# Performance work log

Measured on AMD Instinct MI355X. Metric: run time of the kernel, lower is better.

The kernel has to match this reference:

```python
import jax, jax.numpy as jnp
import numpy as np

STRIDE, PADDING, EPS = 2, 1, 1e-5


def setup_inputs() -> dict:
    key = jax.random.key(0)
    k1, k2, k3 = jax.random.split(key, 3)
    C_in, C_out, K = 64, 64, 4
    x = jax.random.normal(k1, (32, C_in, 64, 64), dtype=jnp.float32)
    weight = jax.random.normal(k2, (C_in, C_out, K, K), dtype=jnp.float32) * 0.05  # torch layout (in,out,kh,kw)
    conv_bias = jax.random.normal(k3, (C_out,), dtype=jnp.float32) * 0.02
    gamma = jnp.ones((C_out,), dtype=jnp.float32)
    beta = jnp.zeros((C_out,), dtype=jnp.float32)
    running_mean = jnp.zeros((C_out,), dtype=jnp.float32)
    running_var = jnp.ones((C_out,), dtype=jnp.float32)
    return {"x": x, "weight": weight, "conv_bias": conv_bias, "gamma": gamma,
            "beta": beta, "running_mean": running_mean, "running_var": running_var}


def _conv_transpose2d(x, weight, bias, stride, padding):
    # torch.nn.functional.conv_transpose2d equivalent:
    # conv with lhs_dilation=stride, spatially-flipped kernel, in/out axes swapped,
    # and padding k-1-p on each side.
    k = weight.shape[2]
    w_t = jnp.transpose(jnp.flip(weight, (2, 3)), (1, 0, 2, 3))  # (Cout, Cin, k, k)
    pad = k - 1 - padding
    y = jax.lax.conv_general_dilated(
        x, w_t,
        window_strides=(1, 1),
        padding=[(pad, pad), (pad, pad)],
        lhs_dilation=(stride, stride),
        dimension_numbers=("NCHW", "OIHW", "NCHW"),
    )
    return y + bias[None, :, None, None]


def reference(x, weight, conv_bias, gamma, beta, running_mean, running_var):
    # ConvTranspose2d
    y = _conv_transpose2d(x, weight, conv_bias, STRIDE, PADDING)  # [N,C,128,128]
    # BatchNorm2d (inference, running stats)
    scale = gamma * jax.lax.rsqrt(running_var + EPS)
    y = (y - running_mean[None, :, None, None]) * scale[None, :, None, None] + beta[None, :, None, None]
    # Softmax over channel dim
    y = jax.nn.softmax(y, axis=1)
    # MaxPool2d(k=2, s=2): H,W are even, so reshape-max is exact
    N, C, H, W = y.shape
    y = y.reshape(N, C, H // 2, 2, W // 2, 2).max(axis=(3, 5))  # [N,C,64,64]
    return y
```

## Files before the change

### kernel.cpp

```cpp
#include <hip/hip_runtime.h>
#include <hip/hip_bf16.h>
#include <math.h>


typedef __attribute__((ext_vector_type(8))) short short8;
typedef __attribute__((ext_vector_type(4))) float floatx4;

#define COLS 66

__device__ ushort g_wfrag[4 * 8 * 4 * 64 * 8];
__device__ float g_aff[64];

__device__ __forceinline__ ushort f2bf(float f) {
  union { float f; unsigned u; } v; v.f = f;
  unsigned r = v.u + 0x7FFF + ((v.u >> 16) & 1);
  return (ushort)(r >> 16);
}

__global__ __launch_bounds__(256) void prep_kernel(
    const float* __restrict__ w, const float* __restrict__ bias,
    const float* __restrict__ gamma, const float* __restrict__ beta,
    const float* __restrict__ mean, const float* __restrict__ var) {
  int t = blockIdx.x * 256 + threadIdx.x;
  int cin0 = (t >> 6) * 2;
  int cout = t & 63;
  int nt = cout >> 4, b15 = cout & 15;
  int q = (cin0 & 31) >> 3;
  int j = cin0 & 7;
  int ksq = cin0 >> 5;
  float A = gamma[cout] * rsqrtf(var[cout] + 1e-5f);

  const float4* p0 = (const float4*)&w[(cin0 * 64 + cout) * 16];
  const float4* p1 = (const float4*)&w[((cin0 + 1) * 64 + cout) * 16];
  float a[16], b[16];
  {
    float4 f0 = p0[0], f1 = p0[1], f2 = p0[2], f3 = p0[3];
    a[0]=f0.x; a[1]=f0.y; a[2]=f0.z; a[3]=f0.w; a[4]=f1.x; a[5]=f1.y; a[6]=f1.z; a[7]=f1.w;
    a[8]=f2.x; a[9]=f2.y; a[10]=f2.z; a[11]=f2.w; a[12]=f3.x; a[13]=f3.y; a[14]=f3.z; a[15]=f3.w;
    float4 g0 = p1[0], g1 = p1[1], g2 = p1[2], g3 = p1[3];
    b[0]=g0.x; b[1]=g0.y; b[2]=g0.z; b[3]=g0.w; b[4]=g1.x; b[5]=g1.y; b[6]=g1.z; b[7]=g1.w;
    b[8]=g2.x; b[9]=g2.y; b[10]=g2.z; b[11]=g2.w; b[12]=g3.x; b[13]=g3.y; b[14]=g3.z; b[15]=g3.w;
  }
#pragma unroll
  for (int kh = 0; kh < 4; ++kh)
#pragma unroll
    for (int kw = 0; kw < 4; ++kw) {
      int r = (kh & 1) ? 0 : 1;
      int pp = (kw & 1) ? 0 : 1;
      int c = r * 2 + pp;
      int tap = (kh >> 1) * 2 + (kw >> 1);
      int ks = tap * 2 + ksq;
      unsigned u = (unsigned)f2bf(a[kh * 4 + kw] * A) |
                   ((unsigned)f2bf(b[kh * 4 + kw] * A) << 16);
      *(unsigned*)&g_wfrag[(((c * 8 + ks) * 4 + nt) * 64 + q * 16 + b15) * 8 + j] = u;
    }

  if (t < 64) {
    float Ai = gamma[t] * rsqrtf(var[t] + 1e-5f);
    g_aff[t] = (bias[t] - mean[t]) * Ai + beta[t];
  }
}

__global__ __launch_bounds__(256, 4) void fused_kernel(const float* __restrict__ x,
                                                       float* __restrict__ out) {
  __shared__ ushort xs[4 * COLS * 64];

  const int tid  = threadIdx.x;
  const int ph0  = blockIdx.x * 2;
  const int n    = blockIdx.y;
  const int wave = tid >> 6;
  const int lane = tid & 63;
  const int b15  = lane & 15;
  const int q    = lane >> 4;
  const int wr   = wave >> 1;
  const int wc   = wave & 1;

  for (int e = tid; e < 4 * 16 * 16; e += 256) {
    int iw4 = e & 15;
    int c4  = (e >> 4) & 15;
    int row = e >> 8;
    int ih  = ph0 - 1 + row;
    float4 v0 = {0.f, 0.f, 0.f, 0.f}, v1 = v0, v2 = v0, v3 = v0;
    if (ih >= 0 && ih < 64) {
      const float* xp = x + ((n * 64 + c4 * 4) * 64 + ih) * 64 + iw4 * 4;
      v0 = *(const float4*)xp;          v1 = *(const float4*)(xp + 4096);
      v2 = *(const float4*)(xp + 8192); v3 = *(const float4*)(xp + 12288);
    }
    int chunk = c4 >> 1, half4 = (c4 & 1) * 4;
    float cc[4][4] = {{v0.x, v1.x, v2.x, v3.x}, {v0.y, v1.y, v2.y, v3.y},
                      {v0.z, v1.z, v2.z, v3.z}, {v0.w, v1.w, v2.w, v3.w}};
#pragma unroll
    for (int ii = 0; ii < 4; ++ii) {
      int col = iw4 * 4 + ii + 1;
      __hip_bfloat162 lo = __float22bfloat162_rn({cc[ii][0], cc[ii][1]});
      __hip_bfloat162 hi = __float22bfloat162_rn({cc[ii][2], cc[ii][3]});
      ushort4 pk = {*(ushort*)&lo.x, *(ushort*)&lo.y, *(ushort*)&hi.x, *(ushort*)&hi.y};
      *(ushort4*)&xs[(row * COLS + col) * 64 + ((chunk ^ (col & 7)) * 8) + half4] = pk;
    }
  }
  for (int e = tid; e < 4 * 2 * 16; e += 256) {
    int c4 = e & 15, side = (e >> 4) & 1, row = e >> 5;
    int col = side ? 65 : 0;
    int chunk = c4 >> 1, half4 = (c4 & 1) * 4;
    ushort4 z; z.x = z.y = z.z = z.w = 0;
    *(ushort4*)&xs[(row * COLS + col) * 64 + ((chunk ^ (col & 7)) * 8) + half4] = z;
  }
  __syncthreads();

  float Dc[4];
#pragma unroll
  for (int nt = 0; nt < 4; ++nt) Dc[nt] = g_aff[nt * 16 + b15];

  floatx4 pooled[8];
#pragma unroll
  for (int i = 0; i < 8; ++i) pooled[i] = (floatx4){0.f, 0.f, 0.f, 0.f};

  short8 bfA[4], bfB[4];
  {
    const short8* wf = (const short8*)g_wfrag;
#pragma unroll
    for (int nt = 0; nt < 4; ++nt) bfA[nt] = wf[nt * 64 + lane];
  }

  for (int c = 0; c < 4; ++c) {
    const int r = c >> 1, p = c & 1;
    floatx4 acc[8];
#pragma unroll
    for (int i = 0; i < 8; ++i) acc[i] = (floatx4){0.f, 0.f, 0.f, 0.f};

#pragma unroll
    for (int ks = 0; ks < 8; ++ks) {
      short8* cur = (ks & 1) ? bfB : bfA;
      short8* nxt = (ks & 1) ? bfA : bfB;
      if (ks < 7) {
        const short8* wf = (const short8*)g_wfrag + (c * 8 + ks + 1) * 256;
#pragma unroll
        for (int nt = 0; nt < 4; ++nt) nxt[nt] = wf[nt * 64 + lane];
      } else if (c < 3) {
        const short8* wf = (const short8*)g_wfrag + (c + 1) * 8 * 256;
#pragma unroll
        for (int nt = 0; nt < 4; ++nt) nxt[nt] = wf[nt * 64 + lane];
      }
      const int a = ks >> 2, b = (ks >> 1) & 1;
      const int hrow = wr + (r ? (a ? 1 : 2) : (a ? 0 : 1));
      const int dx   = p ? (b ? 0 : 1) : (b ? -1 : 0);
      const int chunk = (ks & 1) * 4 + q;
      short8 af[2];
#pragma unroll
      for (int mt = 0; mt < 2; ++mt) {
        int col = wc * 32 + mt * 16 + b15 + dx + 1;
        af[mt] = *(const short8*)&xs[(hrow * COLS + col) * 64 + ((chunk ^ (col & 7)) * 8)];
      }
#pragma unroll
      for (int nt = 0; nt < 4; ++nt)
#pragma unroll
        for (int mt = 0; mt < 2; ++mt)
          acc[mt * 4 + nt] =
              __builtin_amdgcn_mfma_f32_16x16x32_bf16(af[mt], cur[nt], acc[mt * 4 + nt], 0, 0, 0);
    }

#pragma unroll
    for (int mt = 0; mt < 2; ++mt) {
      float sm[4] = {0.f, 0.f, 0.f, 0.f};
#pragma unroll
      for (int nt = 0; nt < 4; ++nt)
#pragma unroll
        for (int reg = 0; reg < 4; ++reg) {
          float e = __expf(acc[mt * 4 + nt][reg] + Dc[nt]);
          acc[mt * 4 + nt][reg] = e;
          sm[reg] += e;
        }
#pragma unroll
      for (int reg = 0; reg < 4; ++reg) {
        sm[reg] += __shfl_xor(sm[reg], 1, 64);
        sm[reg] += __shfl_xor(sm[reg], 2, 64);
        sm[reg] += __shfl_xor(sm[reg], 4, 64);
        sm[reg] += __shfl_xor(sm[reg], 8, 64);
        sm[reg] = 1.0f / sm[reg];
      }
#pragma unroll
      for (int nt = 0; nt < 4; ++nt)
#pragma unroll
        for (int reg = 0; reg < 4; ++reg)
          pooled[mt * 4 + nt][reg] =
              fmaxf(pooled[mt * 4 + nt][reg], acc[mt * 4 + nt][reg] * sm[reg]);
    }
  }

  __syncthreads();
  float* red = (float*)xs;
#pragma unroll
  for (int mt = 0; mt < 2; ++mt)
#pragma unroll
    for (int nt = 0; nt < 4; ++nt)
#pragma unroll
      for (int reg = 0; reg < 4; ++reg)
        red[(wr * 64 + nt * 16 + b15) * 66 + wc * 32 + mt * 16 + q * 4 + reg] =
            pooled[mt * 4 + nt][reg];
  __syncthreads();
  for (int e = tid; e < 4096; e += 256) {
    int pw2  = e & 31;
    int cout = (e >> 5) & 63;
    int rl   = e >> 11;
    float2 val = *(float2*)&red[(rl * 64 + cout) * 66 + pw2 * 2];
    *(float2*)&out[((n * 64 + cout) * 64 + (ph0 + rl)) * 64 + pw2 * 2] = val;
  }
}

extern "C" void kernel_launch(void* const* d_in, const int* in_sizes, int n_in,
                              void* d_out, int out_size, void* d_ws, size_t ws_size,
                              hipStream_t stream) {
  const float* x     = (const float*)d_in[0];
  const float* w     = (const float*)d_in[1];
  const float* bias  = (const float*)d_in[2];
  const float* gamma = (const float*)d_in[3];
  const float* beta  = (const float*)d_in[4];
  const float* mean  = (const float*)d_in[5];
  const float* var   = (const float*)d_in[6];
  float* out = (float*)d_out;

  prep_kernel<<<8, 256, 0, stream>>>(w, bias, gamma, beta, mean, var);
  dim3 grid(32, 32);
  fused_kernel<<<grid, 256, 0, stream>>>(x, out);
}
```

Before: 120.4 us.

## Split parity classes across waves, one pooled row per block, atomic LDS max

Each block now handles one pooled output row with 8 waves, and each wave pair owns one of the four output parity classes instead of looping over them. Max pooling across waves goes through workgroup-scoped float atomic max in LDS. Edge columns are masked rather than padded. Several smaller changes come with it: log2(e) is folded into the weights and affine term so exp2 can be used, DPP replaces the shuffle reductions, a native bf16 pack conversion is used, and the bias is preloaded into the accumulators. The aim is more parallelism and less serial per-wave work, at the cost of LDS atomics and more redundant input staging per output row.

```diff
diff --git a/kernel.cpp b/kernel.cpp
--- a/kernel.cpp
+++ b/kernel.cpp
@@ -5,11 +5,13 @@
 
 typedef __attribute__((ext_vector_type(8))) short short8;
 typedef __attribute__((ext_vector_type(4))) float floatx4;
-
-#define COLS 66
+typedef __attribute__((ext_vector_type(2))) unsigned uint2v;
+typedef __attribute__((ext_vector_type(4))) unsigned uint4v;
 
 __device__ ushort g_wfrag[4 * 8 * 4 * 64 * 8];
 __device__ float g_aff[64];
+
+#define L2E 1.44269504088896340736f
 
 __device__ __forceinline__ ushort f2bf(float f) {
   union { float f; unsigned u; } v; v.f = f;
@@ -28,7 +30,7 @@
   int q = (cin0 & 31) >> 3;
   int j = cin0 & 7;
   int ksq = cin0 >> 5;
-  float A = gamma[cout] * rsqrtf(var[cout] + 1e-5f);
+  float Aw = gamma[cout] * rsqrtf(var[cout] + 1e-5f) * L2E;
 
   const float4* p0 = (const float4*)&w[(cin0 * 64 + cout) * 16];
   const float4* p1 = (const float4*)&w[((cin0 + 1) * 64 + cout) * 16];
@@ -50,36 +52,80 @@
       int c = r * 2 + pp;
       int tap = (kh >> 1) * 2 + (kw >> 1);
       int ks = tap * 2 + ksq;
-      unsigned u = (unsigned)f2bf(a[kh * 4 + kw] * A) |
-                   ((unsigned)f2bf(b[kh * 4 + kw] * A) << 16);
+      unsigned u = (unsigned)f2bf(a[kh * 4 + kw] * Aw) |
+                   ((unsigned)f2bf(b[kh * 4 + kw] * Aw) << 16);
       *(unsigned*)&g_wfrag[(((c * 8 + ks) * 4 + nt) * 64 + q * 16 + b15) * 8 + j] = u;
     }
 
   if (t < 64) {
-    float Ai = gamma[t] * rsqrtf(var[t] + 1e-5f);
-    g_aff[t] = (bias[t] - mean[t]) * Ai + beta[t];
-  }
-}
-
-__global__ __launch_bounds__(256, 4) void fused_kernel(const float* __restrict__ x,
+    float A0 = gamma[t] * rsqrtf(var[t] + 1e-5f);
+    g_aff[t] = ((bias[t] - mean[t]) * A0 + beta[t]) * L2E;
+  }
+}
+
+__device__ __forceinline__ unsigned cvtpk(float a, float b) {
+  unsigned r;
+  asm("v_cvt_pk_bf16_f32 %0, %1, %2" : "=v"(r) : "v"(a), "v"(b));
+  return r;
+}
+
+__device__ __forceinline__ short8 and8(short8 v, unsigned m) {
+  union { short8 s; uint4v u; } x;
+  x.s = v;
+  x.u &= m;
+  return x.s;
+}
+
+template <int CTRL>
+__device__ __forceinline__ float dpp_add(float v) {
+  unsigned t = (unsigned)__builtin_amdgcn_update_dpp(
+      0, (int)__float_as_uint(v), CTRL, 0xF, 0xF, true);
+  return v + __uint_as_float(t);
+}
+
+__device__ __forceinline__ float sum16(float v) {
+  v = dpp_add<0xB1>(v);
+  v = dpp_add<0x4E>(v);
+  v = dpp_add<0x141>(v);
+  v = dpp_add<0x140>(v);
+  return v;
+}
+
+__device__ __forceinline__ float fexp2(float x) {
+#if __has_builtin(__builtin_amdgcn_exp2f)
+  return __builtin_amdgcn_exp2f(x);
+#else
+  return exp2f(x);
+#endif
+}
+
+__global__ __launch_bounds__(512, 6) void fused_kernel(const float* __restrict__ x,
                                                        float* __restrict__ out) {
-  __shared__ ushort xs[4 * COLS * 64];
+  __shared__ __align__(16) ushort xs[3 * 64 * 64];
+  __shared__ __align__(16) float red[64 * 64];
 
   const int tid  = threadIdx.x;
-  const int ph0  = blockIdx.x * 2;
+  const int ph   = blockIdx.x;
   const int n    = blockIdx.y;
   const int wave = tid >> 6;
   const int lane = tid & 63;
   const int b15  = lane & 15;
   const int q    = lane >> 4;
-  const int wr   = wave >> 1;
   const int wc   = wave & 1;
-
-  for (int e = tid; e < 4 * 16 * 16; e += 256) {
+  const int c    = wave >> 1;
+  const int r    = c >> 1, p = c & 1;
+
+  {
+    float4 z = {0.f, 0.f, 0.f, 0.f};
+    *(float4*)&red[tid * 8] = z;
+    *(float4*)&red[tid * 8 + 4] = z;
+  }
+
+  for (int e = tid; e < 768; e += 512) {
     int iw4 = e & 15;
     int c4  = (e >> 4) & 15;
     int row = e >> 8;
-    int ih  = ph0 - 1 + row;
+    int ih  = ph - 1 + row;
     float4 v0 = {0.f, 0.f, 0.f, 0.f}, v1 = v0, v2 = v0, v3 = v0;
     if (ih >= 0 && ih < 64) {
       const float* xp = x + ((n * 64 + c4 * 4) * 64 + ih) * 64 + iw4 * 4;
@@ -91,119 +137,99 @@
                       {v0.z, v1.z, v2.z, v3.z}, {v0.w, v1.w, v2.w, v3.w}};
 #pragma unroll
     for (int ii = 0; ii < 4; ++ii) {
-      int col = iw4 * 4 + ii + 1;
-      __hip_bfloat162 lo = __float22bfloat162_rn({cc[ii][0], cc[ii][1]});
-      __hip_bfloat162 hi = __float22bfloat162_rn({cc[ii][2], cc[ii][3]});
-      ushort4 pk = {*(ushort*)&lo.x, *(ushort*)&lo.y, *(ushort*)&hi.x, *(ushort*)&hi.y};
-      *(ushort4*)&xs[(row * COLS + col) * 64 + ((chunk ^ (col & 7)) * 8) + half4] = pk;
-    }
-  }
-  for (int e = tid; e < 4 * 2 * 16; e += 256) {
-    int c4 = e & 15, side = (e >> 4) & 1, row = e >> 5;
-    int col = side ? 65 : 0;
-    int chunk = c4 >> 1, half4 = (c4 & 1) * 4;
-    ushort4 z; z.x = z.y = z.z = z.w = 0;
-    *(ushort4*)&xs[(row * COLS + col) * 64 + ((chunk ^ (col & 7)) * 8) + half4] = z;
-  }
-  __syncthreads();
+      int col = iw4 * 4 + ii;
+      uint2v pk = {cvtpk(cc[ii][0], cc[ii][1]), cvtpk(cc[ii][2], cc[ii][3])};
+      *(uint2v*)&xs[(row * 64 + col) * 64 + ((chunk ^ (col & 7)) * 8) + half4] = pk;
+    }
+  }
 
   float Dc[4];
 #pragma unroll
   for (int nt = 0; nt < 4; ++nt) Dc[nt] = g_aff[nt * 16 + b15];
 
-  floatx4 pooled[8];
-#pragma unroll
-  for (int i = 0; i < 8; ++i) pooled[i] = (floatx4){0.f, 0.f, 0.f, 0.f};
+  const unsigned m_b0 = (p == 1 && wc == 1 && b15 == 15) ? 0u : ~0u;
+  const unsigned m_b1 = (p == 0 && wc == 0 && b15 == 0) ? 0u : ~0u;
+
+  int A_[2][2][2];
+#pragma unroll
+  for (int mt = 0; mt < 2; ++mt)
+#pragma unroll
+    for (int b = 0; b < 2; ++b) {
+      int col = (wc * 32 + mt * 16 + b15 + (b ? p - 1 : p)) & 63;
+#pragma unroll
+      for (int par = 0; par < 2; ++par)
+        A_[mt][b][par] = r * 4096 + col * 64 + (((par * 4 + q) ^ (col & 7)) * 8);
+    }
 
   short8 bfA[4], bfB[4];
   {
-    const short8* wf = (const short8*)g_wfrag;
+    const short8* wf = (const short8*)g_wfrag + (c * 8) * 256;
 #pragma unroll
     for (int nt = 0; nt < 4; ++nt) bfA[nt] = wf[nt * 64 + lane];
   }
-
-  for (int c = 0; c < 4; ++c) {
-    const int r = c >> 1, p = c & 1;
-    floatx4 acc[8];
-#pragma unroll
-    for (int i = 0; i < 8; ++i) acc[i] = (floatx4){0.f, 0.f, 0.f, 0.f};
-
-#pragma unroll
-    for (int ks = 0; ks < 8; ++ks) {
-      short8* cur = (ks & 1) ? bfB : bfA;
-      short8* nxt = (ks & 1) ? bfA : bfB;
-      if (ks < 7) {
-        const short8* wf = (const short8*)g_wfrag + (c * 8 + ks + 1) * 256;
-#pragma unroll
-        for (int nt = 0; nt < 4; ++nt) nxt[nt] = wf[nt * 64 + lane];
-      } else if (c < 3) {
-        const short8* wf = (const short8*)g_wfrag + (c + 1) * 8 * 256;
-#pragma unroll
-        for (int nt = 0; nt < 4; ++nt) nxt[nt] = wf[nt * 64 + lane];
+  __syncthreads();
+
+  floatx4 acc[8];
+#pragma unroll
+  for (int nt = 0; nt < 4; ++nt) {
+    acc[nt]     = (floatx4){Dc[nt], Dc[nt], Dc[nt], Dc[nt]};
+    acc[4 + nt] = (floatx4){Dc[nt], Dc[nt], Dc[nt], Dc[nt]};
+  }
+
+#pragma unroll
+  for (int ks = 0; ks < 8; ++ks) {
+    const int a = ks >> 2, b = (ks >> 1) & 1, par = ks & 1;
+    short8* cur = (ks & 1) ? bfB : bfA;
+    short8* nxt = (ks & 1) ? bfA : bfB;
+    if (ks < 7) {
+      const short8* wf = (const short8*)g_wfrag + (c * 8 + ks + 1) * 256;
+#pragma unroll
+      for (int nt = 0; nt < 4; ++nt) nxt[nt] = wf[nt * 64 + lane];
+    }
+    const int ho = a ? 0 : 4096;
+    short8 af0 = *(const short8*)&xs[A_[0][b][par] + ho];
+    short8 af1 = *(const short8*)&xs[A_[1][b][par] + ho];
+    if (b == 0) af1 = and8(af1, m_b0);
+    else        af0 = and8(af0, m_b1);
+#pragma unroll
+    for (int nt = 0; nt < 4; ++nt) {
+      acc[nt]     = __builtin_amdgcn_mfma_f32_16x16x32_bf16(af0, cur[nt], acc[nt], 0, 0, 0);
+      acc[4 + nt] = __builtin_amdgcn_mfma_f32_16x16x32_bf16(af1, cur[nt], acc[4 + nt], 0, 0, 0);
+    }
+  }
+
+#pragma unroll
+  for (int mt = 0; mt < 2; ++mt) {
+    float sm[4] = {0.f, 0.f, 0.f, 0.f};
+#pragma unroll
+    for (int nt = 0; nt < 4; ++nt)
+#pragma unroll
+      for (int reg = 0; reg < 4; ++reg) {
+        float e = fexp2(acc[mt * 4 + nt][reg]);
+        acc[mt * 4 + nt][reg] = e;
+        sm[reg] += e;
       }
-      const int a = ks >> 2, b = (ks >> 1) & 1;
-      const int hrow = wr + (r ? (a ? 1 : 2) : (a ? 0 : 1));
-      const int dx   = p ? (b ? 0 : 1) : (b ? -1 : 0);
-      const int chunk = (ks & 1) * 4 + q;
-      short8 af[2];
-#pragma unroll
-      for (int mt = 0; mt < 2; ++mt) {
-        int col = wc * 32 + mt * 16 + b15 + dx + 1;
-        af[mt] = *(const short8*)&xs[(hrow * COLS + col) * 64 + ((chunk ^ (col & 7)) * 8)];
-      }
-#pragma unroll
-      for (int nt = 0; nt < 4; ++nt)
-#pragma unroll
-        for (int mt = 0; mt < 2; ++mt)
-          acc[mt * 4 + nt] =
-              __builtin_amdgcn_mfma_f32_16x16x32_bf16(af[mt], cur[nt], acc[mt * 4 + nt], 0, 0, 0);
-    }
-
-#pragma unroll
-    for (int mt = 0; mt < 2; ++mt) {
-      float sm[4] = {0.f, 0.f, 0.f, 0.f};
-#pragma unroll
-      for (int nt = 0; nt < 4; ++nt)
-#pragma unroll
-        for (int reg = 0; reg < 4; ++reg) {
-          float e = __expf(acc[mt * 4 + nt][reg] + Dc[nt]);
-          acc[mt * 4 + nt][reg] = e;
-          sm[reg] += e;
-        }
-#pragma unroll
-      for (int reg = 0; reg < 4; ++reg) {
-        sm[reg] += __shfl_xor(sm[reg], 1, 64);
-        sm[reg] += __shfl_xor(sm[reg], 2, 64);
-        sm[reg] += __shfl_xor(sm[reg], 4, 64);
-        sm[reg] += __shfl_xor(sm[reg], 8, 64);
-        sm[reg] = 1.0f / sm[reg];
-      }
-#pragma unroll
-      for (int nt = 0; nt < 4; ++nt)
-#pragma unroll
-        for (int reg = 0; reg < 4; ++reg)
-          pooled[mt * 4 + nt][reg] =
-              fmaxf(pooled[mt * 4 + nt][reg], acc[mt * 4 + nt][reg] * sm[reg]);
-    }
-  }
-
+#pragma unroll
+    for (int reg = 0; reg < 4; ++reg)
+      sm[reg] = __builtin_amdgcn_rcpf(sum16(sm[reg]));
+    const int qb = wc * 8 + mt * 4 + q;
+#pragma unroll
+    for (int nt = 0; nt < 4; ++nt) {
+      int cout = nt * 16 + b15;
+      int idx = cout * 64 + ((qb ^ (cout & 7)) << 2);
+#pragma unroll
+      for (int reg = 0; reg < 4; ++reg)
+        __hip_atomic_fetch_max(&red[idx + reg], acc[mt * 4 + nt][reg] * sm[reg],
+                               __ATOMIC_RELAXED, __HIP_MEMORY_SCOPE_WORKGROUP);
+    }
+  }
   __syncthreads();
-  float* red = (float*)xs;
-#pragma unroll
-  for (int mt = 0; mt < 2; ++mt)
-#pragma unroll
-    for (int nt = 0; nt < 4; ++nt)
-#pragma unroll
-      for (int reg = 0; reg < 4; ++reg)
-        red[(wr * 64 + nt * 16 + b15) * 66 + wc * 32 + mt * 16 + q * 4 + reg] =
-            pooled[mt * 4 + nt][reg];
-  __syncthreads();
-  for (int e = tid; e < 4096; e += 256) {
+
+  for (int e = tid; e < 2048; e += 512) {
     int pw2  = e & 31;
-    int cout = (e >> 5) & 63;
-    int rl   = e >> 11;
-    float2 val = *(float2*)&red[(rl * 64 + cout) * 66 + pw2 * 2];
-    *(float2*)&out[((n * 64 + cout) * 64 + (ph0 + rl)) * 64 + pw2 * 2] = val;
+    int cout = e >> 5;
+    float2 val = *(float2*)&red[cout * 64 + (((pw2 >> 1) ^ (cout & 7)) << 2) + (pw2 & 1) * 2];
+    *(float2*)&out[((n * 64 + cout) * 64 + ph) * 64 + pw2 * 2] = val;
   }
 }
 
@@ -220,6 +246,6 @@
   float* out = (float*)d_out;
 
   prep_kernel<<<8, 256, 0, stream>>>(w, bias, gamma, beta, mean, var);
-  dim3 grid(32, 32);
-  fused_kernel<<<grid, 256, 0, stream>>>(x, out);
-}
+  dim3 grid(64, 32);
+  fused_kernel<<<grid, 512, 0, stream>>>(x, out);
+}
```

After: 129.0 us. 1.07x slower.
